# Performance work log

Hardware: AMD Instinct MI355X
Metric: run time of the kernel (lower is better)

## Reference

```python
import jax, jax.numpy as jnp
import numpy as np

B, H, T, K, V = 2, 8, 2048, 128, 128


def setup_inputs() -> dict:
    key = jax.random.key(0)
    k1, k2, k3, k4, k5 = jax.random.split(key, 5)
    return {
        "q": jax.random.normal(k1, (B, H, T, K), dtype=jnp.float32),
        "k": jax.random.normal(k2, (B, H, T, K), dtype=jnp.float32),
        "v": jax.random.normal(k3, (B, H, T, V), dtype=jnp.float32),
        "i_gate": jax.random.normal(k4, (B, H, T), dtype=jnp.float32),
        "f_gate": jax.random.normal(k5, (B, H, T), dtype=jnp.float32),
    }


def reference(q, k, v, i_gate, f_gate):
    # Stabilized parallel mLSTM (same math as the chunked Triton kernel,
    # expressed in natural-log base instead of base-2).
    Bq, Hq, Tq, Kd = q.shape
    scale = Kd ** -0.5
    logf = jax.nn.log_sigmoid(f_gate)                      # [B,H,T]
    fc = jnp.cumsum(logf, axis=-1)                         # cumulative forget logits
    # log decay matrix: logD[t,s] = i[s] + (fc[t] - fc[s]) for s <= t
    logD = fc[..., :, None] - fc[..., None, :] + i_gate[..., None, :]  # [B,H,T,T]
    mask = jnp.tril(jnp.ones((Tq, Tq), dtype=bool))
    logD_masked = jnp.where(mask, logD, -jnp.inf)
    m = jnp.max(logD_masked, axis=-1)                      # row-wise stabilizer [B,H,T]
    D = jnp.where(mask, jnp.exp(logD - m[..., None]), 0.0) # stabilized decay matrix
    S = jnp.einsum("bhtk,bhsk->bhts", q, k) * scale * D    # gated scores
    norm = jnp.maximum(jnp.abs(jnp.sum(S, axis=-1)), jnp.exp(-m))  # [B,H,T]
    h = jnp.einsum("bhts,bhsv->bhtv", S, v) / norm[..., None]
    return h
```

## Files before the change

kernel.cpp:

```cpp
#include <hip/hip_runtime.h>

#define T_SEQ 2048
#define DHEAD 128
#define NBH 16
#define SCALE 0.08838834764831845f

typedef unsigned short u16;
typedef unsigned int u32;
typedef u16 u16x4 __attribute__((ext_vector_type(4)));
typedef u16 u16x8 __attribute__((ext_vector_type(8)));
typedef u32 u32x2 __attribute__((ext_vector_type(2)));
typedef short s16x4 __attribute__((ext_vector_type(4)));
typedef __bf16 bf16x8 __attribute__((ext_vector_type(8)));
typedef float f32x4 __attribute__((ext_vector_type(4)));

__device__ __forceinline__ u16 f2bfu(float x) {
  union { float f; unsigned u; } c; c.f = x;
  unsigned u = c.u;
  u = u + 0x7FFFu + ((u >> 16) & 1u);
  return (u16)(u >> 16);
}

__device__ __forceinline__ u32 packbf2(float lo, float hi) {
  return (u32)f2bfu(lo) | ((u32)f2bfu(hi) << 16);
}

__device__ __forceinline__ bf16x8 ldsFrag(const u16* p) {
  u16x8 t = *(const u16x8*)p;
  return __builtin_bit_cast(bf16x8, t);
}

__device__ __forceinline__ f32x4 mfma16x16x16bf16(s16x4 a, s16x4 b, f32x4 c) {
#if __has_builtin(__builtin_amdgcn_mfma_f32_16x16x16bf16_1k)
  return __builtin_amdgcn_mfma_f32_16x16x16bf16_1k(a, b, c, 0, 0, 0);
#else
  asm("v_mfma_f32_16x16x16_bf16 %0, %1, %2, %0" : "+v"(c) : "v"(a), "v"(b));
  return c;
#endif
}

__device__ __forceinline__ void gld_lds16(const void* g, void* l) {
  __builtin_amdgcn_global_load_lds(
      (__attribute__((address_space(1))) const unsigned int*)g,
      (__attribute__((address_space(3))) unsigned int*)l, 16, 0, 0);
}

__global__ __launch_bounds__(256) void gate_scan_kernel(
    const float* __restrict__ ig, const float* __restrict__ fg,
    float* __restrict__ a_out, float* __restrict__ c_out,
    float* __restrict__ fc_out)
{
  const int bh  = blockIdx.x;
  const int tid = threadIdx.x;
  const int base = bh * T_SEQ + tid * 8;
  __shared__ float sbuf[256];

  float lf[8];
  float run = 0.f;
#pragma unroll
  for (int j = 0; j < 8; ++j) {
    float x  = fg[base + j];
    float ls = fminf(x, 0.f) - log1pf(expf(-fabsf(x)));
    run += ls; lf[j] = run;
  }
  sbuf[tid] = run; __syncthreads();
  for (int off = 1; off < 256; off <<= 1) {
    float t = (tid >= off) ? sbuf[tid - off] : 0.f;
    __syncthreads();
    sbuf[tid] += t;
    __syncthreads();
  }
  const float excl = (tid > 0) ? sbuf[tid - 1] : 0.f;
  __syncthreads();

  float fc[8], cm[8];
  float runm = -INFINITY;
#pragma unroll
  for (int j = 0; j < 8; ++j) {
    fc[j] = excl + lf[j];
    fc_out[base + j] = fc[j];
    float av = ig[base + j] - fc[j];
    a_out[base + j] = av;
    runm = fmaxf(runm, av);
    cm[j] = runm;
  }
  sbuf[tid] = runm; __syncthreads();
  for (int off = 1; off < 256; off <<= 1) {
    float t = (tid >= off) ? sbuf[tid - off] : -INFINITY;
    __syncthreads();
    sbuf[tid] = fmaxf(sbuf[tid], t);
    __syncthreads();
  }
  const float exclm = (tid > 0) ? sbuf[tid - 1] : -INFINITY;
#pragma unroll
  for (int j = 0; j < 8; ++j) {
    c_out[base + j] = fmaxf(exclm, cm[j]);
  }
}

__global__ __launch_bounds__(256) void cvt_k_kernel(
    const float* __restrict__ src, const float* __restrict__ ag,
    const float* __restrict__ cg, u16* __restrict__ dst)
{
  const int i = (blockIdx.x * 256 + threadIdx.x) * 4;
  const int bhs = i >> 7;
  const float sc = __expf(ag[bhs] - cg[bhs | 63]);
  const float4 x = *(const float4*)(src + i);
  u16x4 p;
  p[0] = f2bfu(x.x * sc); p[1] = f2bfu(x.y * sc);
  p[2] = f2bfu(x.z * sc); p[3] = f2bfu(x.w * sc);
  *(u16x4*)(dst + i) = p;
}

__global__ __launch_bounds__(256) void cvt_vt_kernel(
    const float* __restrict__ v, u16* __restrict__ vt)
{
  const int bh = blockIdx.y, kt = blockIdx.x, tid = threadIdx.x;
  __shared__ __align__(16) u16 L[128 * 72];
  const int n0 = (tid & 31) * 4, k0 = (tid >> 5) * 8;
  const float* vp = v + ((size_t)bh * T_SEQ + kt * 64 + k0) * DHEAD + n0;
  u16 tv[4][8];
#pragma unroll
  for (int rr = 0; rr < 8; ++rr) {
    const float4 x = *(const float4*)(vp + rr * DHEAD);
    tv[0][rr] = f2bfu(x.x); tv[1][rr] = f2bfu(x.y);
    tv[2][rr] = f2bfu(x.z); tv[3][rr] = f2bfu(x.w);
  }
#pragma unroll
  for (int j = 0; j < 4; ++j) {
    u16x8 p;
#pragma unroll
    for (int rr = 0; rr < 8; ++rr) p[rr] = tv[j][rr];
    *(u16x8*)(&L[(n0 + j) * 72 + k0]) = p;
  }
  __syncthreads();
  const int row = tid >> 1, s0 = (tid & 1) * 32;
  u16* op = vt + ((size_t)bh * DHEAD + row) * T_SEQ + kt * 64 + s0;
#pragma unroll
  for (int i = 0; i < 4; ++i)
    *(u16x8*)(op + i * 8) = *(const u16x8*)(&L[row * 72 + s0 + i * 8]);
}

template <bool FAST>
__global__ __launch_bounds__(512, 1) void mlstm_fwd_kernel(
    const float* __restrict__ qg, const float* __restrict__ kxg,
    const float* __restrict__ vg,
    const u16* __restrict__ kbf, const u16* __restrict__ vtbf,
    const float* __restrict__ ag, const float* __restrict__ cg,
    const float* __restrict__ fcg, float* __restrict__ out)
{
  const int bx = (int)blockIdx.x;
  const int bh = bx & 15, p = bx >> 4;
  const int tid = (int)threadIdx.x;
  const int w8 = tid >> 6, lane = tid & 63;
  const int quad = lane >> 4, l16 = lane & 15;

  const int qsel = w8 >> 2;
  const int kg4  = w8 & 3;
  const int qt   = qsel ? p : (31 - p);
  const int nST  = 32 - p;
  const int qrow0 = qt * 64;

  __shared__ __align__(16) unsigned char SM[68096];

  const size_t hoff = (size_t)bh * T_SEQ * DHEAD;
  const int goff = bh * T_SEQ;

  bf16x8 qf[16];
#pragma unroll
  for (int nt = 0; nt < 4; ++nt) {
    const float* qp = qg + hoff + (size_t)(qrow0 + nt * 16 + l16) * DHEAD + quad * 8;
#pragma unroll
    for (int kc = 0; kc < 4; ++kc) {
      const float4 x0 = *(const float4*)(qp + kc * 32);
      const float4 x1 = *(const float4*)(qp + kc * 32 + 4);
      u16x8 t;
      t[0] = f2bfu(x0.x); t[1] = f2bfu(x0.y); t[2] = f2bfu(x0.z); t[3] = f2bfu(x0.w);
      t[4] = f2bfu(x1.x); t[5] = f2bfu(x1.y); t[6] = f2bfu(x1.z); t[7] = f2bfu(x1.w);
      qf[nt * 4 + kc] = __builtin_bit_cast(bf16x8, t);
    }
  }
  const float cmax = cg[goff + qt * 64 + 63];

  f32x4 oa[8][4];
#pragma unroll
  for (int mt = 0; mt < 8; ++mt)
#pragma unroll
    for (int nt = 0; nt < 4; ++nt) oa[mt][nt] = (f32x4){0.f, 0.f, 0.f, 0.f};
  float rsacc[4] = {0.f, 0.f, 0.f, 0.f};

  auto stage = [&](int st) {
    const int b = st & 1;
    u16* KbL = (u16*)(SM + b * 16384);
    u16* VbL = (u16*)(SM + 32768 + b * 16384);
    if (FAST) {
      const u16* ks = kbf + ((size_t)goff + st * 64) * DHEAD;
      const u16* vs = vtbf + (size_t)bh * DHEAD * T_SEQ + st * 64;
#pragma unroll
      for (int j = 0; j < 2; ++j) {
        const int B = (w8 * 2 + j) * 64 + lane;
        { const int key = B >> 4; const int db = (B & 15) ^ (key & 7);
          gld_lds16(ks + (size_t)key * DHEAD + db * 8, KbL + (w8 * 2 + j) * 512); }
        { const int n = B >> 3; const int kb = (B & 7) ^ (n & 7);
          gld_lds16(vs + (size_t)n * T_SEQ + kb * 8, VbL + (w8 * 2 + j) * 512); }
      }
    } else {
      const float ct = cg[goff + st * 64 + 63];
      const float* kp = kxg + hoff + (size_t)(st * 64) * DHEAD;
      const float* vp = vg + hoff + (size_t)(st * 64) * DHEAD;
#pragma unroll
      for (int j = 0; j < 2; ++j) {
        const int B = (w8 * 2 + j) * 64 + lane;
        { const int key = B >> 4; const int db = (B & 15) ^ (key & 7);
          const float sc = __expf(ag[goff + st * 64 + key] - ct);
          const float4 x0 = *(const float4*)(kp + (size_t)key * DHEAD + db * 8);
          const float4 x1 = *(const float4*)(kp + (size_t)key * DHEAD + db * 8 + 4);
          u16x8 pk;
          pk[0] = f2bfu(x0.x * sc); pk[1] = f2bfu(x0.y * sc);
          pk[2] = f2bfu(x0.z * sc); pk[3] = f2bfu(x0.w * sc);
          pk[4] = f2bfu(x1.x * sc); pk[5] = f2bfu(x1.y * sc);
          pk[6] = f2bfu(x1.z * sc); pk[7] = f2bfu(x1.w * sc);
          *(u16x8*)(KbL + B * 8) = pk; }
        { const int n = B >> 3; const int kb = (B & 7) ^ (n & 7);
          u16x8 pw;
#pragma unroll
          for (int rr = 0; rr < 8; ++rr)
            pw[rr] = f2bfu(vp[(size_t)(kb * 8 + rr) * DHEAD + n]);
          *(u16x8*)(VbL + B * 8) = pw; }
      }
    }
  };

  stage(0);
  __syncthreads();

  const int keyA = kg4 * 16 + l16;
  const int ksw  = l16 & 7;
  const int kbu  = kg4 * 2 + (quad >> 1);
  const int kofs = (quad & 1) * 4;

  for (int st = 0; st < nST; ++st) {
    const int b = st & 1;
    if (st + 1 < nST) stage(st + 1);

    if (st <= qt) {
      const u16* KbL = (const u16*)(SM + b * 16384);
      const u16* VbL = (const u16*)(SM + 32768 + b * 16384);

      f32x4 sa[4];
#pragma unroll
      for (int nt = 0; nt < 4; ++nt) sa[nt] = (f32x4){0.f, 0.f, 0.f, 0.f};
#pragma unroll
      for (int kc = 0; kc < 4; ++kc) {
        const bf16x8 kf = ldsFrag(KbL + keyA * 128 + (((kc * 4 + quad) ^ ksw) * 8));
        sa[0] = __builtin_amdgcn_mfma_f32_16x16x32_bf16(kf, qf[0 * 4 + kc], sa[0], 0, 0, 0);
        sa[1] = __builtin_amdgcn_mfma_f32_16x16x32_bf16(kf, qf[1 * 4 + kc], sa[1], 0, 0, 0);
        sa[2] = __builtin_amdgcn_mfma_f32_16x16x32_bf16(kf, qf[2 * 4 + kc], sa[2], 0, 0, 0);
        sa[3] = __builtin_amdgcn_mfma_f32_16x16x32_bf16(kf, qf[3 * 4 + kc], sa[3], 0, 0, 0);
      }

      const float etile = SCALE * __expf(cg[goff + st * 64 + 63] - cmax);
      const bool diag = (st == qt);

      s16x4 pfr[4];
#pragma unroll
      for (int nt = 0; nt < 4; ++nt) {
        float x0 = sa[nt][0] * etile, x1 = sa[nt][1] * etile;
        float x2 = sa[nt][2] * etile, x3 = sa[nt][3] * etile;
        if (diag) {
          const int qr = nt * 16 + l16, kb0 = kg4 * 16 + quad * 4;
          if (kb0 + 0 > qr) x0 = 0.f;
          if (kb0 + 1 > qr) x1 = 0.f;
          if (kb0 + 2 > qr) x2 = 0.f;
          if (kb0 + 3 > qr) x3 = 0.f;
        }
        rsacc[nt] += (x0 + x1) + (x2 + x3);
        pfr[nt] = __builtin_bit_cast(s16x4, (u32x2){packbf2(x0, x1), packbf2(x2, x3)});
      }

#pragma unroll
      for (int mt = 0; mt < 8; ++mt) {
        const int vd = mt * 16 + l16;
        const s16x4 va = *(const s16x4*)(VbL + vd * 64 + ((kbu ^ (vd & 7)) * 8) + kofs);
        oa[mt][0] = mfma16x16x16bf16(va, pfr[0], oa[mt][0]);
        oa[mt][1] = mfma16x16x16bf16(va, pfr[1], oa[mt][1]);
        oa[mt][2] = mfma16x16x16bf16(va, pfr[2], oa[mt][2]);
        oa[mt][3] = mfma16x16x16bf16(va, pfr[3], oa[mt][3]);
      }
    }
    __syncthreads();
  }

  float rst[4];
#pragma unroll
  for (int nt = 0; nt < 4; ++nt) {
    float x = rsacc[nt];
    x += __shfl_xor(x, 16, 64);
    x += __shfl_xor(x, 32, 64);
    rst[nt] = x;
  }
  float* rshp = (float*)(SM + 66048);
  if (lane < 16) {
#pragma unroll
    for (int nt = 0; nt < 4; ++nt)
      rshp[qsel * 256 + kg4 * 64 + nt * 16 + lane] = rst[nt];
  }
  __syncthreads();

  float inv[4] = {0.f, 0.f, 0.f, 0.f};
  if (kg4 == 3) {
#pragma unroll
    for (int nt = 0; nt < 4; ++nt) {
      const int row = nt * 16 + l16;
      const float tot = rshp[qsel * 256 + row] + rshp[qsel * 256 + 64 + row]
                      + rshp[qsel * 256 + 128 + row] + rshp[qsel * 256 + 192 + row];
      const float nf = __expf(-(cmax + fcg[goff + qrow0 + row]));
      inv[nt] = 1.f / fmaxf(fabsf(tot), nf);
    }
  }

  float* osh = (float*)SM;
  const int obase = qsel * 64 * 129;
  for (int r = 0; r < 4; ++r) {
    if (kg4 == r) {
#pragma unroll
      for (int mt = 0; mt < 8; ++mt)
#pragma unroll
        for (int nt = 0; nt < 4; ++nt)
#pragma unroll
          for (int rg = 0; rg < 4; ++rg) {
            const int row = nt * 16 + l16;
            const int vd = mt * 16 + quad * 4 + rg;
            const int ad = obase + row * 129 + vd;
            float v = oa[mt][nt][rg];
            if (r > 0) v += osh[ad];
            if (r == 3) v *= inv[nt];
            osh[ad] = v;
          }
    }
    __syncthreads();
  }

  {
    const int col = tid & 31;
    const int rg0 = tid >> 5;
#pragma unroll
    for (int i = 0; i < 8; ++i) {
      const int ra = rg0 + 16 * i;
      const int tile = ra >> 6, row = ra & 63;
      const int qtt = tile ? p : (31 - p);
      const float* lp = osh + (tile * 64 + row) * 129 + col * 4;
      float4 v; v.x = lp[0]; v.y = lp[1]; v.z = lp[2]; v.w = lp[3];
      *(float4*)(out + hoff + (size_t)(qtt * 64 + row) * DHEAD + col * 4) = v;
    }
  }
}

extern "C" void kernel_launch(void* const* d_in, const int* in_sizes, int n_in,
                              void* d_out, int out_size, void* d_ws, size_t ws_size,
                              hipStream_t stream) {
  const float* q  = (const float*)d_in[0];
  const float* k  = (const float*)d_in[1];
  const float* v  = (const float*)d_in[2];
  const float* ig = (const float*)d_in[3];
  const float* fg = (const float*)d_in[4];

  const size_t gate_bytes = (size_t)3 * NBH * T_SEQ * sizeof(float);
  const size_t kv_elems   = (size_t)NBH * T_SEQ * DHEAD;
  const bool fast = ws_size >= gate_bytes + 2 * kv_elems * sizeof(u16);

  float* a_ws  = (float*)d_ws;
  float* c_ws  = a_ws + NBH * T_SEQ;
  float* fc_ws = c_ws + NBH * T_SEQ;
  u16* kbf  = (u16*)((char*)d_ws + gate_bytes);
  u16* vtbf = kbf + kv_elems;

  gate_scan_kernel<<<dim3(NBH), dim3(256), 0, stream>>>(ig, fg, a_ws, c_ws, fc_ws);
  if (fast) {
    cvt_k_kernel<<<dim3((unsigned)(kv_elems / 1024)), dim3(256), 0, stream>>>(
        k, a_ws, c_ws, kbf);
    cvt_vt_kernel<<<dim3(T_SEQ / 64, NBH), dim3(256), 0, stream>>>(v, vtbf);
    mlstm_fwd_kernel<true><<<dim3(256), dim3(512), 0, stream>>>(
        q, k, v, kbf, vtbf, a_ws, c_ws, fc_ws, (float*)d_out);
  } else {
    mlstm_fwd_kernel<false><<<dim3(256), dim3(512), 0, stream>>>(
        q, k, v, kbf, vtbf, a_ws, c_ws, fc_ws, (float*)d_out);
  }
}
```

Before: 150.3 us.

## Split paired-tile blocks into one-query-tile blocks with XCD-aware head mapping

Replaces the 512-thread blocks that each processed a short and a long query tile together with 256-thread blocks that each own a single query tile. The launch grows to 512 blocks, the block index is remapped so both heads sharing an XCD land together with longest tiles scheduled first, and launch bounds allow two blocks per CU. This is meant to drop the wasted staging iterations of the paired scheme and improve load balance and L2 locality. In exchange each block stages K/V for only one query tile, so shared-memory reuse per load is halved and there are more synchronisation points per useful MFMA.

```diff
diff --git a/kernel.cpp b/kernel.cpp
--- a/kernel.cpp
+++ b/kernel.cpp
@@ -142,7 +142,7 @@
 }
 
 template <bool FAST>
-__global__ __launch_bounds__(512, 1) void mlstm_fwd_kernel(
+__global__ __launch_bounds__(256, 2) void mlstm_fwd_kernel(
     const float* __restrict__ qg, const float* __restrict__ kxg,
     const float* __restrict__ vg,
     const u16* __restrict__ kbf, const u16* __restrict__ vtbf,
@@ -150,18 +150,16 @@
     const float* __restrict__ fcg, float* __restrict__ out)
 {
   const int bx = (int)blockIdx.x;
-  const int bh = bx & 15, p = bx >> 4;
+  const int xcd = bx & 7, j = bx >> 3;
+  const int bh = (xcd << 1) | (j & 1);
+  const int qt = 31 - (j >> 1);
   const int tid = (int)threadIdx.x;
-  const int w8 = tid >> 6, lane = tid & 63;
+  const int w4 = tid >> 6, lane = tid & 63;
   const int quad = lane >> 4, l16 = lane & 15;
 
-  const int qsel = w8 >> 2;
-  const int kg4  = w8 & 3;
-  const int qt   = qsel ? p : (31 - p);
-  const int nST  = 32 - p;
   const int qrow0 = qt * 64;
 
-  __shared__ __align__(16) unsigned char SM[68096];
+  __shared__ __align__(16) unsigned char SM[66560];
 
   const size_t hoff = (size_t)bh * T_SEQ * DHEAD;
   const int goff = bh * T_SEQ;
@@ -197,20 +195,20 @@
       const u16* ks = kbf + ((size_t)goff + st * 64) * DHEAD;
       const u16* vs = vtbf + (size_t)bh * DHEAD * T_SEQ + st * 64;
 #pragma unroll
-      for (int j = 0; j < 2; ++j) {
-        const int B = (w8 * 2 + j) * 64 + lane;
+      for (int jj = 0; jj < 4; ++jj) {
+        const int B = (w4 * 4 + jj) * 64 + lane;
         { const int key = B >> 4; const int db = (B & 15) ^ (key & 7);
-          gld_lds16(ks + (size_t)key * DHEAD + db * 8, KbL + (w8 * 2 + j) * 512); }
+          gld_lds16(ks + (size_t)key * DHEAD + db * 8, KbL + (w4 * 4 + jj) * 512); }
         { const int n = B >> 3; const int kb = (B & 7) ^ (n & 7);
-          gld_lds16(vs + (size_t)n * T_SEQ + kb * 8, VbL + (w8 * 2 + j) * 512); }
+          gld_lds16(vs + (size_t)n * T_SEQ + kb * 8, VbL + (w4 * 4 + jj) * 512); }
       }
     } else {
       const float ct = cg[goff + st * 64 + 63];
       const float* kp = kxg + hoff + (size_t)(st * 64) * DHEAD;
       const float* vp = vg + hoff + (size_t)(st * 64) * DHEAD;
 #pragma unroll
-      for (int j = 0; j < 2; ++j) {
-        const int B = (w8 * 2 + j) * 64 + lane;
+      for (int jj = 0; jj < 4; ++jj) {
+        const int B = (w4 * 4 + jj) * 64 + lane;
         { const int key = B >> 4; const int db = (B & 15) ^ (key & 7);
           const float sc = __expf(ag[goff + st * 64 + key] - ct);
           const float4 x0 = *(const float4*)(kp + (size_t)key * DHEAD + db * 8);
@@ -234,59 +232,57 @@
   stage(0);
   __syncthreads();
 
-  const int keyA = kg4 * 16 + l16;
+  const int keyA = w4 * 16 + l16;
   const int ksw  = l16 & 7;
-  const int kbu  = kg4 * 2 + (quad >> 1);
+  const int kbu  = w4 * 2 + (quad >> 1);
   const int kofs = (quad & 1) * 4;
 
-  for (int st = 0; st < nST; ++st) {
+  for (int st = 0; st <= qt; ++st) {
     const int b = st & 1;
-    if (st + 1 < nST) stage(st + 1);
-
-    if (st <= qt) {
-      const u16* KbL = (const u16*)(SM + b * 16384);
-      const u16* VbL = (const u16*)(SM + 32768 + b * 16384);
-
-      f32x4 sa[4];
-#pragma unroll
-      for (int nt = 0; nt < 4; ++nt) sa[nt] = (f32x4){0.f, 0.f, 0.f, 0.f};
-#pragma unroll
-      for (int kc = 0; kc < 4; ++kc) {
-        const bf16x8 kf = ldsFrag(KbL + keyA * 128 + (((kc * 4 + quad) ^ ksw) * 8));
-        sa[0] = __builtin_amdgcn_mfma_f32_16x16x32_bf16(kf, qf[0 * 4 + kc], sa[0], 0, 0, 0);
-        sa[1] = __builtin_amdgcn_mfma_f32_16x16x32_bf16(kf, qf[1 * 4 + kc], sa[1], 0, 0, 0);
-        sa[2] = __builtin_amdgcn_mfma_f32_16x16x32_bf16(kf, qf[2 * 4 + kc], sa[2], 0, 0, 0);
-        sa[3] = __builtin_amdgcn_mfma_f32_16x16x32_bf16(kf, qf[3 * 4 + kc], sa[3], 0, 0, 0);
+    if (st < qt) stage(st + 1);
+
+    const u16* KbL = (const u16*)(SM + b * 16384);
+    const u16* VbL = (const u16*)(SM + 32768 + b * 16384);
+
+    f32x4 sa[4];
+#pragma unroll
+    for (int nt = 0; nt < 4; ++nt) sa[nt] = (f32x4){0.f, 0.f, 0.f, 0.f};
+#pragma unroll
+    for (int kc = 0; kc < 4; ++kc) {
+      const bf16x8 kf = ldsFrag(KbL + keyA * 128 + (((kc * 4 + quad) ^ ksw) * 8));
+      sa[0] = __builtin_amdgcn_mfma_f32_16x16x32_bf16(kf, qf[0 * 4 + kc], sa[0], 0, 0, 0);
+      sa[1] = __builtin_amdgcn_mfma_f32_16x16x32_bf16(kf, qf[1 * 4 + kc], sa[1], 0, 0, 0);
+      sa[2] = __builtin_amdgcn_mfma_f32_16x16x32_bf16(kf, qf[2 * 4 + kc], sa[2], 0, 0, 0);
+      sa[3] = __builtin_amdgcn_mfma_f32_16x16x32_bf16(kf, qf[3 * 4 + kc], sa[3], 0, 0, 0);
+    }
+
+    const float etile = SCALE * __expf(cg[goff + st * 64 + 63] - cmax);
+    const bool diag = (st == qt);
+
+    s16x4 pfr[4];
+#pragma unroll
+    for (int nt = 0; nt < 4; ++nt) {
+      float x0 = sa[nt][0] * etile, x1 = sa[nt][1] * etile;
+      float x2 = sa[nt][2] * etile, x3 = sa[nt][3] * etile;
+      if (diag) {
+        const int qr = nt * 16 + l16, kb0 = w4 * 16 + quad * 4;
+        if (kb0 + 0 > qr) x0 = 0.f;
+        if (kb0 + 1 > qr) x1 = 0.f;
+        if (kb0 + 2 > qr) x2 = 0.f;
+        if (kb0 + 3 > qr) x3 = 0.f;
       }
-
-      const float etile = SCALE * __expf(cg[goff + st * 64 + 63] - cmax);
-      const bool diag = (st == qt);
-
-      s16x4 pfr[4];
-#pragma unroll
-      for (int nt = 0; nt < 4; ++nt) {
-        float x0 = sa[nt][0] * etile, x1 = sa[nt][1] * etile;
-        float x2 = sa[nt][2] * etile, x3 = sa[nt][3] * etile;
-        if (diag) {
-          const int qr = nt * 16 + l16, kb0 = kg4 * 16 + quad * 4;
-          if (kb0 + 0 > qr) x0 = 0.f;
-          if (kb0 + 1 > qr) x1 = 0.f;
-          if (kb0 + 2 > qr) x2 = 0.f;
-          if (kb0 + 3 > qr) x3 = 0.f;
-        }
-        rsacc[nt] += (x0 + x1) + (x2 + x3);
-        pfr[nt] = __builtin_bit_cast(s16x4, (u32x2){packbf2(x0, x1), packbf2(x2, x3)});
-      }
-
-#pragma unroll
-      for (int mt = 0; mt < 8; ++mt) {
-        const int vd = mt * 16 + l16;
-        const s16x4 va = *(const s16x4*)(VbL + vd * 64 + ((kbu ^ (vd & 7)) * 8) + kofs);
-        oa[mt][0] = mfma16x16x16bf16(va, pfr[0], oa[mt][0]);
-        oa[mt][1] = mfma16x16x16bf16(va, pfr[1], oa[mt][1]);
-        oa[mt][2] = mfma16x16x16bf16(va, pfr[2], oa[mt][2]);
-        oa[mt][3] = mfma16x16x16bf16(va, pfr[3], oa[mt][3]);
-      }
+      rsacc[nt] += (x0 + x1) + (x2 + x3);
+      pfr[nt] = __builtin_bit_cast(s16x4, (u32x2){packbf2(x0, x1), packbf2(x2, x3)});
+    }
+
+#pragma unroll
+    for (int mt = 0; mt < 8; ++mt) {
+      const int vd = mt * 16 + l16;
+      const s16x4 va = *(const s16x4*)(VbL + vd * 64 + ((kbu ^ (vd & 7)) * 8) + kofs);
+      oa[mt][0] = mfma16x16x16bf16(va, pfr[0], oa[mt][0]);
+      oa[mt][1] = mfma16x16x16bf16(va, pfr[1], oa[mt][1]);
+      oa[mt][2] = mfma16x16x16bf16(va, pfr[2], oa[mt][2]);
+      oa[mt][3] = mfma16x16x16bf16(va, pfr[3], oa[mt][3]);
     }
     __syncthreads();
   }
@@ -299,30 +295,28 @@
     x += __shfl_xor(x, 32, 64);
     rst[nt] = x;
   }
-  float* rshp = (float*)(SM + 66048);
+  float* rshp = (float*)(SM + 65536);
   if (lane < 16) {
 #pragma unroll
     for (int nt = 0; nt < 4; ++nt)
-      rshp[qsel * 256 + kg4 * 64 + nt * 16 + lane] = rst[nt];
+      rshp[w4 * 64 + nt * 16 + lane] = rst[nt];
   }
   __syncthreads();
 
   float inv[4] = {0.f, 0.f, 0.f, 0.f};
-  if (kg4 == 3) {
+  if (w4 == 3) {
 #pragma unroll
     for (int nt = 0; nt < 4; ++nt) {
       const int row = nt * 16 + l16;
-      const float tot = rshp[qsel * 256 + row] + rshp[qsel * 256 + 64 + row]
-                      + rshp[qsel * 256 + 128 + row] + rshp[qsel * 256 + 192 + row];
+      const float tot = rshp[row] + rshp[64 + row] + rshp[128 + row] + rshp[192 + row];
       const float nf = __expf(-(cmax + fcg[goff + qrow0 + row]));
       inv[nt] = 1.f / fmaxf(fabsf(tot), nf);
     }
   }
 
   float* osh = (float*)SM;
-  const int obase = qsel * 64 * 129;
   for (int r = 0; r < 4; ++r) {
-    if (kg4 == r) {
+    if (w4 == r) {
 #pragma unroll
       for (int mt = 0; mt < 8; ++mt)
 #pragma unroll
@@ -331,7 +325,7 @@
           for (int rg = 0; rg < 4; ++rg) {
             const int row = nt * 16 + l16;
             const int vd = mt * 16 + quad * 4 + rg;
-            const int ad = obase + row * 129 + vd;
+            const int ad = row * 129 + vd;
             float v = oa[mt][nt][rg];
             if (r > 0) v += osh[ad];
             if (r == 3) v *= inv[nt];
@@ -346,12 +340,10 @@
     const int rg0 = tid >> 5;
 #pragma unroll
     for (int i = 0; i < 8; ++i) {
-      const int ra = rg0 + 16 * i;
-      const int tile = ra >> 6, row = ra & 63;
-      const int qtt = tile ? p : (31 - p);
-      const float* lp = osh + (tile * 64 + row) * 129 + col * 4;
+      const int row = rg0 + 8 * i;
+      const float* lp = osh + row * 129 + col * 4;
       float4 v; v.x = lp[0]; v.y = lp[1]; v.z = lp[2]; v.w = lp[3];
-      *(float4*)(out + hoff + (size_t)(qtt * 64 + row) * DHEAD + col * 4) = v;
+      *(float4*)(out + hoff + (size_t)(qrow0 + row) * DHEAD + col * 4) = v;
     }
   }
 }
@@ -380,10 +372,10 @@
     cvt_k_kernel<<<dim3((unsigned)(kv_elems / 1024)), dim3(256), 0, stream>>>(
         k, a_ws, c_ws, kbf);
     cvt_vt_kernel<<<dim3(T_SEQ / 64, NBH), dim3(256), 0, stream>>>(v, vtbf);
-    mlstm_fwd_kernel<true><<<dim3(256), dim3(512), 0, stream>>>(
+    mlstm_fwd_kernel<true><<<dim3(512), dim3(256), 0, stream>>>(
         q, k, v, kbf, vtbf, a_ws, c_ws, fc_ws, (float*)d_out);
   } else {
-    mlstm_fwd_kernel<false><<<dim3(256), dim3(512), 0, stream>>>(
+    mlstm_fwd_kernel<false><<<dim3(512), dim3(256), 0, stream>>>(
         q, k, v, kbf, vtbf, a_ws, c_ws, fc_ws, (float*)d_out);
   }
 }
```

Result: slower. 174.1 us (+15.8%).
